# Kernel tuning notes

Measured on AMD Instinct MI355X. Metric: run time of the kernel, lower is better.

Reference implementation:

```python
import jax, jax.numpy as jnp
import numpy as np

Cl, Nl, Cv, Nv, M = 32, 128, 8, 64, 500000


def _sample1d(line, g):
    # line: [C, N]; g in [-1,1]; align_corners=True, zeros padding
    C, N = line.shape
    ix = (g + 1.0) * 0.5 * (N - 1)
    i0 = jnp.floor(ix)
    w = ix - i0
    i0 = i0.astype(jnp.int32)
    def gth(i, wt):
        valid = (i >= 0) & (i < N)
        return line[:, jnp.clip(i, 0, N - 1)] * (wt * valid)
    return (gth(i0, 1.0 - w) + gth(i0 + 1, w)).T  # [M, C]


def _sample2d(plane, gx, gy):
    # plane: [C, H, W]; grid x -> W axis, y -> H axis (torch grid_sample convention)
    C, H, W = plane.shape
    ix = (gx + 1.0) * 0.5 * (W - 1)
    iy = (gy + 1.0) * 0.5 * (H - 1)
    x0 = jnp.floor(ix); y0 = jnp.floor(iy)
    wx = ix - x0; wy = iy - y0
    x0 = x0.astype(jnp.int32); y0 = y0.astype(jnp.int32)
    flat = plane.reshape(C, -1)
    def gth(xi, yi, wt):
        valid = (xi >= 0) & (xi < W) & (yi >= 0) & (yi < H)
        idx = jnp.clip(yi, 0, H - 1) * W + jnp.clip(xi, 0, W - 1)
        return flat[:, idx] * (wt * valid)
    out = (gth(x0, y0, (1 - wx) * (1 - wy)) + gth(x0 + 1, y0, wx * (1 - wy))
           + gth(x0, y0 + 1, (1 - wx) * wy) + gth(x0 + 1, y0 + 1, wx * wy))
    return out.T  # [M, C]


def _sample3d(vol, gx, gy, gz):
    # vol: [C, D, H, W]; grid (x,y,z) -> (W,H,D) axes
    C, D, H, W = vol.shape
    ix = (gx + 1.0) * 0.5 * (W - 1)
    iy = (gy + 1.0) * 0.5 * (H - 1)
    iz = (gz + 1.0) * 0.5 * (D - 1)
    x0 = jnp.floor(ix); y0 = jnp.floor(iy); z0 = jnp.floor(iz)
    wx = ix - x0; wy = iy - y0; wz = iz - z0
    x0 = x0.astype(jnp.int32); y0 = y0.astype(jnp.int32); z0 = z0.astype(jnp.int32)
    flat = vol.reshape(C, -1)
    out = 0.0
    for dz in (0, 1):
        for dy in (0, 1):
            for dx in (0, 1):
                xi, yi, zi = x0 + dx, y0 + dy, z0 + dz
                wt = ((wx if dx else 1 - wx) * (wy if dy else 1 - wy) * (wz if dz else 1 - wz))
                valid = (xi >= 0) & (xi < W) & (yi >= 0) & (yi < H) & (zi >= 0) & (zi < D)
                idx = (jnp.clip(zi, 0, D - 1) * H + jnp.clip(yi, 0, H - 1)) * W + jnp.clip(xi, 0, W - 1)
                out = out + flat[:, idx] * (wt * valid)
    return out.T  # [M, C]


def setup_inputs() -> dict:
    key = jax.random.key(0)
    ks = jax.random.split(key, 16)
    rng, shift = 0.4, 0.1
    coordinates = jax.random.uniform(ks[0], (1, M, 3), minval=-1.0, maxval=1.0)
    line_x = jax.random.uniform(ks[1], (Cl, Nl)) * rng + shift
    line_y = jax.random.uniform(ks[2], (Cl, Nl)) * rng + shift
    line_z = jax.random.uniform(ks[3], (Cl, Nl)) * rng + shift
    plane_xy = jax.random.normal(ks[4], (Cl, Nl, Nl)) * rng + shift
    plane_yz = jax.random.normal(ks[5], (Cl, Nl, Nl)) * rng + shift
    plane_xz = jax.random.normal(ks[6], (Cl, Nl, Nl)) * rng + shift
    volume = jax.random.normal(ks[7], (Cv, Nv, Nv, Nv)) * rng + shift
    def lin(k, fi, fo):
        k1, k2 = jax.random.split(k)
        lim = 1.0 / np.sqrt(fi)
        return (jax.random.uniform(k1, (fi, fo), minval=-lim, maxval=lim),
                jax.random.uniform(k2, (fo,), minval=-lim, maxval=lim))
    Wx, bx = lin(ks[8], Cl, Cl)
    Wy, by = lin(ks[9], Cl, Cl)
    Wz, bz = lin(ks[10], Cl, Cl)
    W1, b1 = lin(ks[11], Cl + Cv, 128)
    W2, b2 = lin(ks[12], 128, 1)
    return dict(coordinates=coordinates, line_x=line_x, line_y=line_y, line_z=line_z,
                plane_xy=plane_xy, plane_yz=plane_yz, plane_xz=plane_xz, volume=volume,
                Wx=Wx, bx=bx, Wy=Wy, by=by, Wz=Wz, bz=bz, W1=W1, b1=b1, W2=W2, b2=b2)


def reference(coordinates, line_x, line_y, line_z, plane_xy, plane_yz, plane_xz, volume,
              Wx, bx, Wy, by, Wz, bz, W1, b1, W2, b2):
    c = coordinates[0]  # [M, 3], batch squeezed like the torch code
    x, y, z = c[:, 0], c[:, 1], c[:, 2]
    x_e = _sample1d(line_x, x)
    y_e = _sample1d(line_y, y)
    z_e = _sample1d(line_z, z)
    xy_e = _sample2d(plane_xy, x, y)
    yz_e = _sample2d(plane_yz, y, z)
    xz_e = _sample2d(plane_xz, x, z)
    xyz_e = _sample3d(volume, x, y, z)
    phi = lambda e, W, b: jax.nn.relu(e) @ W + b  # Sequential(ReLU, Linear)
    yztran = phi(yz_e, Wx, bx)
    xztran = phi(xz_e, Wy, by)
    xytran = phi(xy_e, Wz, bz)
    xtran = phi(x_e, Wx, bx)
    ytran = phi(y_e, Wy, by)
    ztran = phi(z_e, Wz, bz)
    features = xtran * yztran + ytran * xztran + ztran * xytran
    features = jnp.concatenate([features, xyz_e], axis=-1)  # [M, Cl+Cv]
    h = jax.nn.relu(features @ W1 + b1)
    return h @ W2 + b2  # [M, 1]
```

## Files before the change

### kernel.cpp

```cpp
#include <hip/hip_runtime.h>

typedef unsigned short u16;
typedef u16 u16x8 __attribute__((ext_vector_type(8)));
typedef _Float16 half2 __attribute__((ext_vector_type(2)));
typedef _Float16 h8v __attribute__((ext_vector_type(8)));
typedef float f4v __attribute__((ext_vector_type(4)));

union H8 { h8v v; half2 p[4]; };

static __device__ __forceinline__ float bf2f(u16 u) {
    union { unsigned int i; float f; } v;
    v.i = ((unsigned int)u) << 16;
    return v.f;
}
static __device__ __forceinline__ u16 f2bf(float f) {
    union { float f; unsigned int i; } v;
    v.f = f;
    unsigned int x = v.i;
    x += 0x7fffu + ((x >> 16) & 1u);
    return (u16)(x >> 16);
}
static __device__ __forceinline__ float gld(int dt, const void* p, int i) {
    return dt ? ((const float*)p)[i] : bf2f(((const u16*)p)[i]);
}
static __device__ __forceinline__ int detect_dt(const void* coords) {
    u16 v = ((const u16*)coords)[threadIdx.x & 63];
    int e = (v >> 7) & 0xFF;
    bool inr = (e >= 90) && (e <= 126);
    unsigned long long m = __ballot(inr);
    return (__popcll(m) >= 56) ? 0 : 1;
}
static __device__ __forceinline__ half2 pk(float a, float b) {
    return __builtin_bit_cast(half2, __builtin_amdgcn_cvt_pkrtz(a, b));
}

#define WF_OFF        64u
#define PLANES_S_OFF  34304u
#define VOL_S_OFF     3180032u
#define LINES_S_OFF   7374336u
#define PART_OFF      7398912u
#define TOT_OFF       11593216u
#define ORDER_OFF     11609600u

#define NBUCK 4096
#define HBLOCKS 256


static __device__ __forceinline__ int make_key(int dt, const void* coords, int p) {
    float x = gld(dt, coords, p * 3 + 0);
    float y = gld(dt, coords, p * 3 + 1);
    float z = gld(dt, coords, p * 3 + 2);
    int kx = min(max((int)((x + 1.0f) * 8.0f), 0), 15);
    int ky = min(max((int)((y + 1.0f) * 8.0f), 0), 15);
    int kz = min(max((int)((z + 1.0f) * 8.0f), 0), 15);
    return (kz * 16 + ky) * 16 + kx;
}

static __device__ __forceinline__ void weights_work(
    int dt, int r,
    const void* Wx, const void* bx, const void* Wy, const void* by,
    const void* Wz, const void* bz, const void* W1, const void* b1,
    const void* W2, const void* b2, float* wbase)
{
    _Float16* WtH = (_Float16*)wbase;
    float*    bv  = wbase + 1536;
    _Float16* W1H = (_Float16*)(wbase + 1632);
    float*    b1v = wbase + 5728;
    float*    W2v = wbase + 5856;
    float*    b2v = wbase + 5984;
    if (r < 3072) {
        int m = r >> 10, idx = r & 1023;
        int o = idx >> 5, c = idx & 31;
        const void* s = (m == 0) ? Wx : (m == 1) ? Wy : Wz;
        WtH[r] = (_Float16)gld(dt, s, c * 32 + o);
    } else if (r < 3168) {
        int q2 = r - 3072;
        int m = q2 >> 5, c = q2 & 31;
        const void* s = (m == 0) ? bx : (m == 1) ? by : bz;
        bv[q2] = gld(dt, s, c);
    } else if (r < 11360) {
        int idx = r - 3168;
        int j = idx >> 6, i = idx & 63;
        W1H[idx] = (i < 40) ? (_Float16)gld(dt, W1, i * 128 + j) : (_Float16)0.0f;
    } else if (r < 11488) {
        b1v[r - 11360] = gld(dt, b1, r - 11360);
    } else if (r < 11616) {
        W2v[r - 11488] = gld(dt, W2, r - 11488);
    } else if (r == 11616) {
        b2v[0] = gld(dt, b2, 0);
    }
}

__global__ __launch_bounds__(256) void kp_prep_all(
    const void* __restrict__ coords,
    const void* __restrict__ lx, const void* __restrict__ ly,
    const void* __restrict__ lz,
    const void* __restrict__ pxy, const void* __restrict__ pyz,
    const void* __restrict__ pxz, const void* __restrict__ vol,
    const void* __restrict__ Wx, const void* __restrict__ bx,
    const void* __restrict__ Wy, const void* __restrict__ by,
    const void* __restrict__ Wz, const void* __restrict__ bz,
    const void* __restrict__ W1, const void* __restrict__ b1,
    const void* __restrict__ W2, const void* __restrict__ b2,
    float* __restrict__ wbase,
    u16* __restrict__ planes_s, u16* __restrict__ vol_s,
    u16* __restrict__ lines_s, unsigned int* __restrict__ part, int M)
{
    __shared__ unsigned int lh[NBUCK];
    int dt = detect_dt(coords);
    int blk = blockIdx.x;
    if (blk < 1798) {
        int t = blk * 256 + threadIdx.x;
        u16x8 v;
        if (t < 196608) {
            int o = t * 8;
            int pl = o >> 19;
            int r  = o & 524287;
            int pos = r >> 5, c0 = r & 31;
            const void* src = (pl == 0) ? pxy : (pl == 1) ? pyz : pxz;
#pragma unroll
            for (int i = 0; i < 8; ++i)
                v[i] = dt ? f2bf(((const float*)src)[(c0 + i) * 16384 + pos])
                          : ((const u16*)src)[(c0 + i) * 16384 + pos];
            *(u16x8*)(planes_s + o) = v;
        } else if (t < 458752) {
            int pos = t - 196608;
#pragma unroll
            for (int c = 0; c < 8; ++c)
                v[c] = dt ? f2bf(((const float*)vol)[c * 262144 + pos])
                          : ((const u16*)vol)[c * 262144 + pos];
            *(u16x8*)(vol_s + pos * 8) = v;
        } else {
            int o = (t - 458752) * 8;
            int l = o >> 12, rr = o & 4095;
            int pos = rr >> 5, c0 = rr & 31;
            const void* src = (l == 0) ? lx : (l == 1) ? ly : lz;
#pragma unroll
            for (int i = 0; i < 8; ++i)
                v[i] = dt ? f2bf(((const float*)src)[(c0 + i) * 128 + pos])
                          : ((const u16*)src)[(c0 + i) * 128 + pos];
            *(u16x8*)(lines_s + o) = v;
        }
    } else if (blk < 1844) {
        int r = (blk - 1798) * 256 + threadIdx.x;
        weights_work(dt, r, Wx, bx, Wy, by, Wz, bz, W1, b1, W2, b2, wbase);
    } else {
        int b = blk - 1844;
        for (int i = threadIdx.x; i < NBUCK; i += 256) lh[i] = 0u;
        __syncthreads();
        for (int p = b * 256 + threadIdx.x; p < M; p += HBLOCKS * 256)
            atomicAdd(&lh[make_key(dt, coords, p)], 1u);
        __syncthreads();
        for (int i = threadIdx.x; i < NBUCK; i += 256)
            part[b * NBUCK + i] = lh[i];
    }
}

__global__ __launch_bounds__(64) void kp_colscan(
    unsigned int* __restrict__ part, unsigned int* __restrict__ tot)
{
    int bkt = blockIdx.x * 64 + threadIdx.x;
    unsigned int run = 0;
#pragma unroll 8
    for (int k = 0; k < HBLOCKS; ++k) {
        unsigned int v = part[k * NBUCK + bkt];
        part[k * NBUCK + bkt] = run;
        run += v;
    }
    tot[bkt] = run;
}

__global__ __launch_bounds__(256) void kp_scatter_det(
    const void* __restrict__ coords, const unsigned int* __restrict__ part,
    const unsigned int* __restrict__ tot,
    int* __restrict__ order, int M)
{
    __shared__ unsigned int cnt[NBUCK];
    __shared__ unsigned int psum[256];
    int b = blockIdx.x;
    int t = threadIdx.x;
    unsigned int bs[16];
    unsigned int s = 0;
#pragma unroll
    for (int i = 0; i < 16; ++i) {
        bs[i] = tot[t * 16 + i];
        s += bs[i];
    }
    psum[t] = s;
    __syncthreads();
    if (t == 0) {
        unsigned int run = 0;
        for (int i = 0; i < 256; ++i) { unsigned int v = psum[i]; psum[i] = run; run += v; }
    }
    __syncthreads();
    unsigned int run = psum[t];
#pragma unroll
    for (int i = 0; i < 16; ++i) {
        int bkt = t * 16 + i;
        cnt[bkt] = run + part[b * NBUCK + bkt];
        run += bs[i];
    }
    __syncthreads();
    int dt = detect_dt(coords);
    for (int p = b * 256 + t; p < M; p += HBLOCKS * 256) {
        int key = make_key(dt, coords, p);
        unsigned int pos = atomicAdd(&cnt[key], 1u);
        order[pos] = p;
    }
}

struct Samp { int i0, i1; float w0, w1; };

static __device__ __forceinline__ Samp make_samp(float g, int N) {
    float ix = (g + 1.0f) * 0.5f * (float)(N - 1);
    float fl = floorf(ix);
    float w  = ix - fl;
    int i  = (int)fl;
    int i1 = i + 1;
    float v0 = (i  >= 0 && i  < N) ? 1.0f : 0.0f;
    float v1 = (i1 >= 0 && i1 < N) ? 1.0f : 0.0f;
    Samp s;
    s.w0 = (1.0f - w) * v0;
    s.w1 = w * v1;
    s.i0 = min(max(i, 0), N - 1);
    s.i1 = min(max(i1, 0), N - 1);
    return s;
}

#define MFMA16(a, b, c) __builtin_amdgcn_mfma_f32_16x16x32_f16((a), (b), (c), 0, 0, 0)

#define SRE 40
#define SR2 72

static __device__ __forceinline__ void term_mfma(
    int lane, const u16* __restrict__ Ls, const Samp& sl,
    const u16* __restrict__ Ps, const Samp& sa, const Samp& sb,
    const _Float16* __restrict__ Wt, const float* __restrict__ bvt,
    _Float16* El, _Float16* Ep, float (&feat)[4][2][4])
{
    int q = lane >> 4, l15 = lane & 15;
    const u16x8* l0  = (const u16x8*)(Ls + sl.i0 * 32);
    const u16x8* l1  = (const u16x8*)(Ls + sl.i1 * 32);
    const u16x8* p00 = (const u16x8*)(Ps + (sb.i0 * 128 + sa.i0) * 32);
    const u16x8* p01 = (const u16x8*)(Ps + (sb.i0 * 128 + sa.i1) * 32);
    const u16x8* p10 = (const u16x8*)(Ps + (sb.i1 * 128 + sa.i0) * 32);
    const u16x8* p11 = (const u16x8*)(Ps + (sb.i1 * 128 + sa.i1) * 32);
    float w00 = sb.w0 * sa.w0, w01 = sb.w0 * sa.w1;
    float w10 = sb.w1 * sa.w0, w11 = sb.w1 * sa.w1;
#pragma unroll
    for (int cc = 0; cc < 4; ++cc) {
        u16x8 A0 = l0[cc], A1 = l1[cc];
        u16x8 Q00 = p00[cc], Q01 = p01[cc], Q10 = p10[cc], Q11 = p11[cc];
        H8 hl, hp;
#pragma unroll
        for (int kk = 0; kk < 4; ++kk) {
            int k0 = 2 * kk, k1 = k0 + 1;
            float el0 = sl.w0 * bf2f(A0[k0]) + sl.w1 * bf2f(A1[k0]);
            float el1 = sl.w0 * bf2f(A0[k1]) + sl.w1 * bf2f(A1[k1]);
            float ep0 = w00 * bf2f(Q00[k0]) + w01 * bf2f(Q01[k0])
                      + w10 * bf2f(Q10[k0]) + w11 * bf2f(Q11[k0]);
            float ep1 = w00 * bf2f(Q00[k1]) + w01 * bf2f(Q01[k1])
                      + w10 * bf2f(Q10[k1]) + w11 * bf2f(Q11[k1]);
            hl.p[kk] = pk(fmaxf(el0, 0.0f), fmaxf(el1, 0.0f));
            hp.p[kk] = pk(fmaxf(ep0, 0.0f), fmaxf(ep1, 0.0f));
        }
        *(h8v*)&El[lane * SRE + cc * 8] = hl.v;
        *(h8v*)&Ep[lane * SRE + cc * 8] = hp.v;
    }
    __syncthreads();
    h8v bf0 = *(const h8v*)&Wt[(l15) * 32 + q * 8];
    h8v bf1 = *(const h8v*)&Wt[(16 + l15) * 32 + q * 8];
    float bb0 = bvt[l15], bb1 = bvt[16 + l15];
    f4v c0 = {bb0, bb0, bb0, bb0};
    f4v c1 = {bb1, bb1, bb1, bb1};
#pragma unroll
    for (int mt = 0; mt < 4; ++mt) {
        h8v aL = *(const h8v*)&El[(mt * 16 + l15) * SRE + q * 8];
        h8v aP = *(const h8v*)&Ep[(mt * 16 + l15) * SRE + q * 8];
        f4v ta0 = MFMA16(aL, bf0, c0);
        f4v tb0 = MFMA16(aP, bf0, c0);
        f4v ta1 = MFMA16(aL, bf1, c1);
        f4v tb1 = MFMA16(aP, bf1, c1);
#pragma unroll
        for (int r = 0; r < 4; ++r) {
            feat[mt][0][r] += ta0[r] * tb0[r];
            feat[mt][1][r] += ta1[r] * tb1[r];
        }
    }
    __syncthreads();
}

__global__ __launch_bounds__(64) void kp_main_mfma(
    const void* __restrict__ coords, const int* __restrict__ order,
    const u16* __restrict__ planes_s, const u16* __restrict__ vol_s,
    const u16* __restrict__ lines_s,
    const float* __restrict__ wbase,
    void* __restrict__ out, int M)
{
    __shared__ _Float16 eb[5120];
    __shared__ float res[64];
    int dt = detect_dt(coords);
    const _Float16* WtH = (const _Float16*)wbase;
    const float*    bv  = wbase + 1536;
    const _Float16* W1H = (const _Float16*)(wbase + 1632);
    const float*    b1v = wbase + 5728;
    const float*    W2v = wbase + 5856;
    const float*    b2v = wbase + 5984;

    int lane = threadIdx.x;
    int q = lane >> 4, l15 = lane & 15;
    _Float16* El = eb;
    _Float16* Ep = eb + 2560;
    _Float16* E2 = eb;

    int p = blockIdx.x * 64 + lane;
    p = min(p, M - 1);
    int sp = order[p];

    float x = gld(dt, coords, sp * 3 + 0);
    float y = gld(dt, coords, sp * 3 + 1);
    float z = gld(dt, coords, sp * 3 + 2);

    Samp sx = make_samp(x, 128), sy = make_samp(y, 128), sz = make_samp(z, 128);

    float feat[4][2][4];
#pragma unroll
    for (int mt = 0; mt < 4; ++mt)
#pragma unroll
        for (int n = 0; n < 2; ++n)
#pragma unroll
            for (int r = 0; r < 4; ++r) feat[mt][n][r] = 0.0f;

    term_mfma(lane, lines_s + 0 * 4096, sx, planes_s + 1 * 524288, sy, sz,
              WtH + 0,    bv + 0,  El, Ep, feat);
    term_mfma(lane, lines_s + 1 * 4096, sy, planes_s + 2 * 524288, sx, sz,
              WtH + 1024, bv + 32, El, Ep, feat);
    term_mfma(lane, lines_s + 2 * 4096, sz, planes_s + 0 * 524288, sx, sy,
              WtH + 2048, bv + 64, El, Ep, feat);

#pragma unroll
    for (int mt = 0; mt < 4; ++mt)
#pragma unroll
        for (int n = 0; n < 2; ++n)
#pragma unroll
            for (int r = 0; r < 4; ++r)
                E2[(mt * 16 + q * 4 + r) * SR2 + n * 16 + l15] =
                    (_Float16)feat[mt][n][r];
    {
        Samp vx = make_samp(x, 64), vy = make_samp(y, 64), vz = make_samp(z, 64);
        float vf[8];
#pragma unroll
        for (int c = 0; c < 8; ++c) vf[c] = 0.0f;
#pragma unroll
        for (int corner = 0; corner < 8; ++corner) {
            int dx = corner & 1, dy = (corner >> 1) & 1, dz = corner >> 2;
            int xi = dx ? vx.i1 : vx.i0;
            int yi = dy ? vy.i1 : vy.i0;
            int zi = dz ? vz.i1 : vz.i0;
            float w = (dx ? vx.w1 : vx.w0) * (dy ? vy.w1 : vy.w0) * (dz ? vz.w1 : vz.w0);
            u16x8 v = *(const u16x8*)(vol_s + (((zi * 64) + yi) * 64 + xi) * 8);
#pragma unroll
            for (int c = 0; c < 8; ++c)
                vf[c] = fmaf(w, bf2f(v[c]), vf[c]);
        }
        H8 hv;
#pragma unroll
        for (int k = 0; k < 4; ++k) hv.p[k] = pk(vf[2 * k], vf[2 * k + 1]);
        *(h8v*)&E2[lane * SR2 + 32] = hv.v;
        h8v zz = {};
        *(h8v*)&E2[lane * SR2 + 40] = zz;
        *(h8v*)&E2[lane * SR2 + 48] = zz;
        *(h8v*)&E2[lane * SR2 + 56] = zz;
    }
    __syncthreads();

    h8v af[4][2];
#pragma unroll
    for (int mt = 0; mt < 4; ++mt)
#pragma unroll
        for (int ks = 0; ks < 2; ++ks)
            af[mt][ks] = *(const h8v*)&E2[(mt * 16 + l15) * SR2 + ks * 32 + q * 8];

    float s[4][4];
#pragma unroll
    for (int mt = 0; mt < 4; ++mt)
#pragma unroll
        for (int r = 0; r < 4; ++r) s[mt][r] = 0.0f;

#pragma unroll
    for (int NT = 0; NT < 8; ++NT) {
        int o = NT * 16 + l15;
        h8v b0 = *(const h8v*)&W1H[o * 64 + q * 8];
        h8v b1f = *(const h8v*)&W1H[o * 64 + 32 + q * 8];
        float w2 = W2v[o];
        float bb = b1v[o];
        f4v cinit = {bb, bb, bb, bb};
#pragma unroll
        for (int mt = 0; mt < 4; ++mt) {
            f4v c = MFMA16(af[mt][0], b0, cinit);
            c = MFMA16(af[mt][1], b1f, c);
#pragma unroll
            for (int r = 0; r < 4; ++r)
                s[mt][r] = fmaf(fmaxf(c[r], 0.0f), w2, s[mt][r]);
        }
    }
#pragma unroll
    for (int mt = 0; mt < 4; ++mt)
#pragma unroll
        for (int r = 0; r < 4; ++r) {
            float v = s[mt][r];
            v += __shfl_xor(v, 1);
            v += __shfl_xor(v, 2);
            v += __shfl_xor(v, 4);
            v += __shfl_xor(v, 8);
            s[mt][r] = v;
        }
    if (l15 == 0) {
#pragma unroll
        for (int mt = 0; mt < 4; ++mt)
#pragma unroll
            for (int r = 0; r < 4; ++r)
                res[mt * 16 + q * 4 + r] = s[mt][r];
    }
    __syncthreads();
    float rr = res[lane] + b2v[0];
    if (dt) ((float*)out)[sp] = rr;
    else    ((u16*)out)[sp] = f2bf(rr);
}

__global__ void kp_prep_weights_fb(
    const void* __restrict__ coords,
    const void* __restrict__ Wx, const void* __restrict__ bx,
    const void* __restrict__ Wy, const void* __restrict__ by,
    const void* __restrict__ Wz, const void* __restrict__ bz,
    const void* __restrict__ W1, const void* __restrict__ b1,
    const void* __restrict__ W2, const void* __restrict__ b2,
    float* __restrict__ wbase)
{
    int dt = detect_dt(coords);
    int t = blockIdx.x * blockDim.x + threadIdx.x;
    weights_work(dt, t, Wx, bx, Wy, by, Wz, bz, W1, b1, W2, b2, wbase);
}

__global__ __launch_bounds__(256) void kp_main_direct(
    const void* __restrict__ coords,
    const void* __restrict__ lx, const void* __restrict__ ly, const void* __restrict__ lz,
    const void* __restrict__ pxy, const void* __restrict__ pyz, const void* __restrict__ pxz,
    const void* __restrict__ vol,
    const float* __restrict__ wbase,
    void* __restrict__ out, int M)
{
    int dt = detect_dt(coords);
    const _Float16* WtH = (const _Float16*)wbase;
    const float*    bv  = wbase + 1536;
    const _Float16* W1H = (const _Float16*)(wbase + 1632);
    const float*    b1v = wbase + 5728;
    const float*    W2v = wbase + 5856;
    const float*    b2v = wbase + 5984;

    int p = blockIdx.x * 256 + threadIdx.x;
    p = min(p, M - 1);

    float x = gld(dt, coords, p * 3 + 0);
    float y = gld(dt, coords, p * 3 + 1);
    float z = gld(dt, coords, p * 3 + 2);

    Samp sx = make_samp(x, 128), sy = make_samp(y, 128), sz = make_samp(z, 128);

    float feat[40];
#pragma unroll
    for (int o = 0; o < 40; ++o) feat[o] = 0.0f;

    const void* Ls[3] = {lx, ly, lz};
    const void* Psv[3] = {pyz, pxz, pxy};
    Samp sl3[3] = {sx, sy, sz};
    Samp sa3[3] = {sy, sx, sx};
    Samp sb3[3] = {sz, sz, sy};
#pragma unroll 1
    for (int m = 0; m < 3; ++m) {
        float ta[32], tb[32];
        const float* bvt = bv + m * 32;
        const _Float16* Wt = WtH + m * 1024;
#pragma unroll
        for (int o = 0; o < 32; ++o) { ta[o] = bvt[o]; tb[o] = bvt[o]; }
        Samp sl = sl3[m], sa = sa3[m], sb = sb3[m];
        float w00 = sb.w0 * sa.w0, w01 = sb.w0 * sa.w1;
        float w10 = sb.w1 * sa.w0, w11 = sb.w1 * sa.w1;
        int i00 = sb.i0 * 128 + sa.i0, i01 = sb.i0 * 128 + sa.i1;
        int i10 = sb.i1 * 128 + sa.i0, i11 = sb.i1 * 128 + sa.i1;
#pragma unroll 1
        for (int c = 0; c < 32; ++c) {
            float el = sl.w0 * gld(dt, Ls[m], c * 128 + sl.i0)
                     + sl.w1 * gld(dt, Ls[m], c * 128 + sl.i1);
            float ep = w00 * gld(dt, Psv[m], c * 16384 + i00)
                     + w01 * gld(dt, Psv[m], c * 16384 + i01)
                     + w10 * gld(dt, Psv[m], c * 16384 + i10)
                     + w11 * gld(dt, Psv[m], c * 16384 + i11);
            float r1 = fmaxf(el, 0.0f), r2 = fmaxf(ep, 0.0f);
#pragma unroll
            for (int o = 0; o < 32; ++o) {
                float w = (float)Wt[o * 32 + c];
                ta[o] = fmaf(r1, w, ta[o]);
                tb[o] = fmaf(r2, w, tb[o]);
            }
        }
#pragma unroll
        for (int o = 0; o < 32; ++o) feat[o] = fmaf(ta[o], tb[o], feat[o]);
    }

    Samp vx = make_samp(x, 64), vy = make_samp(y, 64), vz = make_samp(z, 64);
#pragma unroll 1
    for (int corner = 0; corner < 8; ++corner) {
        int dx = corner & 1, dy = (corner >> 1) & 1, dz = corner >> 2;
        int xi = dx ? vx.i1 : vx.i0;
        int yi = dy ? vy.i1 : vy.i0;
        int zi = dz ? vz.i1 : vz.i0;
        float w = (dx ? vx.w1 : vx.w0) * (dy ? vy.w1 : vy.w0) * (dz ? vz.w1 : vz.w0);
        int pos = ((zi * 64) + yi) * 64 + xi;
#pragma unroll
        for (int c = 0; c < 8; ++c)
            feat[32 + c] = fmaf(w, gld(dt, vol, c * 262144 + pos), feat[32 + c]);
    }

    float acc_out = b2v[0];
#pragma unroll 2
    for (int j = 0; j < 128; ++j) {
        float acc = b1v[j];
        const _Float16* wr = W1H + j * 64;
#pragma unroll
        for (int i = 0; i < 40; ++i)
            acc = fmaf(feat[i], (float)wr[i], acc);
        acc_out = fmaf(fmaxf(acc, 0.0f), W2v[j], acc_out);
    }
    if (dt) ((float*)out)[p] = acc_out;
    else    ((u16*)out)[p] = f2bf(acc_out);
}

extern "C" void kernel_launch(void* const* d_in, const int* in_sizes, int n_in,
                              void* d_out, int out_size, void* d_ws, size_t ws_size,
                              hipStream_t stream) {
    const void* coords = d_in[0];
    const void* lx  = d_in[1];
    const void* ly  = d_in[2];
    const void* lz  = d_in[3];
    const void* pxy = d_in[4];
    const void* pyz = d_in[5];
    const void* pxz = d_in[6];
    const void* vol = d_in[7];
    const void* Wx  = d_in[8];
    const void* bx  = d_in[9];
    const void* Wy  = d_in[10];
    const void* by  = d_in[11];
    const void* Wz  = d_in[12];
    const void* bz  = d_in[13];
    const void* W1  = d_in[14];
    const void* b1  = d_in[15];
    const void* W2  = d_in[16];
    const void* b2  = d_in[17];

    int M = in_sizes[0] / 3;

    char* ws = (char*)d_ws;
    float*        wbase    = (float*)(ws + WF_OFF);
    u16*          planes_s = (u16*)(ws + PLANES_S_OFF);
    u16*          vol_s    = (u16*)(ws + VOL_S_OFF);
    u16*          lines_s  = (u16*)(ws + LINES_S_OFF);
    unsigned int* part     = (unsigned int*)(ws + PART_OFF);
    unsigned int* tot      = (unsigned int*)(ws + TOT_OFF);
    int*          order    = (int*)(ws + ORDER_OFF);

    size_t need_sorted = (size_t)ORDER_OFF + (size_t)M * 4u;

    if (ws_size >= need_sorted) {
        kp_prep_all<<<2100, 256, 0, stream>>>(coords, lx, ly, lz, pxy, pyz, pxz, vol,
                                              Wx, bx, Wy, by, Wz, bz, W1, b1, W2, b2,
                                              wbase, planes_s, vol_s, lines_s, part, M);
        kp_colscan<<<64, 64, 0, stream>>>(part, tot);
        kp_scatter_det<<<HBLOCKS, 256, 0, stream>>>(coords, part, tot, order, M);
        int blocks64 = (M + 63) / 64;
        kp_main_mfma<<<blocks64, 64, 0, stream>>>(coords, order, planes_s, vol_s,
                                                  lines_s, wbase, d_out, M);
    } else {
        int blocks = (M + 255) / 256;
        kp_prep_weights_fb<<<46, 256, 0, stream>>>(coords, Wx, bx, Wy, by, Wz, bz,
                                                   W1, b1, W2, b2, wbase);
        kp_main_direct<<<blocks, 256, 0, stream>>>(coords, lx, ly, lz, pxy, pyz, pxz,
                                                   vol, wbase, d_out, M);
    }
}
```

Measured before the change: 203.7 us.

## Scatter coordinates into sorted order, shrink histogram partials, swizzle block order

```diff
diff --git a/kernel.cpp b/kernel.cpp
--- a/kernel.cpp
+++ b/kernel.cpp
@@ -39,21 +39,22 @@
 #define VOL_S_OFF     3180032u
 #define LINES_S_OFF   7374336u
 #define PART_OFF      7398912u
-#define TOT_OFF       11593216u
-#define ORDER_OFF     11609600u
+#define TOT_OFF       9496064u
+#define ORDER_OFF     9512448u
 
 #define NBUCK 4096
 #define HBLOCKS 256
 
 
-static __device__ __forceinline__ int make_key(int dt, const void* coords, int p) {
-    float x = gld(dt, coords, p * 3 + 0);
-    float y = gld(dt, coords, p * 3 + 1);
-    float z = gld(dt, coords, p * 3 + 2);
+static __device__ __forceinline__ int make_key3(float x, float y, float z) {
     int kx = min(max((int)((x + 1.0f) * 8.0f), 0), 15);
     int ky = min(max((int)((y + 1.0f) * 8.0f), 0), 15);
     int kz = min(max((int)((z + 1.0f) * 8.0f), 0), 15);
     return (kz * 16 + ky) * 16 + kx;
+}
+static __device__ __forceinline__ int make_key(int dt, const void* coords, int p) {
+    return make_key3(gld(dt, coords, p * 3 + 0), gld(dt, coords, p * 3 + 1),
+                     gld(dt, coords, p * 3 + 2));
 }
 
 static __device__ __forceinline__ void weights_work(
@@ -104,7 +105,7 @@
     const void* __restrict__ W2, const void* __restrict__ b2,
     float* __restrict__ wbase,
     u16* __restrict__ planes_s, u16* __restrict__ vol_s,
-    u16* __restrict__ lines_s, unsigned int* __restrict__ part, int M)
+    u16* __restrict__ lines_s, u16* __restrict__ part, int M)
 {
     __shared__ unsigned int lh[NBUCK];
     int dt = detect_dt(coords);
@@ -152,28 +153,28 @@
             atomicAdd(&lh[make_key(dt, coords, p)], 1u);
         __syncthreads();
         for (int i = threadIdx.x; i < NBUCK; i += 256)
-            part[b * NBUCK + i] = lh[i];
+            part[b * NBUCK + i] = (u16)lh[i];
     }
 }
 
 __global__ __launch_bounds__(64) void kp_colscan(
-    unsigned int* __restrict__ part, unsigned int* __restrict__ tot)
+    u16* __restrict__ part, unsigned int* __restrict__ tot)
 {
     int bkt = blockIdx.x * 64 + threadIdx.x;
     unsigned int run = 0;
 #pragma unroll 8
     for (int k = 0; k < HBLOCKS; ++k) {
         unsigned int v = part[k * NBUCK + bkt];
-        part[k * NBUCK + bkt] = run;
+        part[k * NBUCK + bkt] = (u16)run;
         run += v;
     }
     tot[bkt] = run;
 }
 
 __global__ __launch_bounds__(256) void kp_scatter_det(
-    const void* __restrict__ coords, const unsigned int* __restrict__ part,
+    const void* __restrict__ coords, const u16* __restrict__ part,
     const unsigned int* __restrict__ tot,
-    int* __restrict__ order, int M)
+    int* __restrict__ order, u16* __restrict__ scoords, int M)
 {
     __shared__ unsigned int cnt[NBUCK];
     __shared__ unsigned int psum[256];
@@ -197,15 +198,24 @@
 #pragma unroll
     for (int i = 0; i < 16; ++i) {
         int bkt = t * 16 + i;
-        cnt[bkt] = run + part[b * NBUCK + bkt];
+        cnt[bkt] = run + (unsigned int)part[b * NBUCK + bkt];
         run += bs[i];
     }
     __syncthreads();
     int dt = detect_dt(coords);
+    const u16* cu = (const u16*)coords;
     for (int p = b * 256 + t; p < M; p += HBLOCKS * 256) {
-        int key = make_key(dt, coords, p);
+        float x = gld(dt, coords, p * 3 + 0);
+        float y = gld(dt, coords, p * 3 + 1);
+        float z = gld(dt, coords, p * 3 + 2);
+        int key = make_key3(x, y, z);
         unsigned int pos = atomicAdd(&cnt[key], 1u);
         order[pos] = p;
+        if (dt == 0) {
+            scoords[pos * 3 + 0] = cu[p * 3 + 0];
+            scoords[pos * 3 + 1] = cu[p * 3 + 1];
+            scoords[pos * 3 + 2] = cu[p * 3 + 2];
+        }
     }
 }
 
@@ -292,6 +302,7 @@
 
 __global__ __launch_bounds__(64) void kp_main_mfma(
     const void* __restrict__ coords, const int* __restrict__ order,
+    const u16* __restrict__ scoords,
     const u16* __restrict__ planes_s, const u16* __restrict__ vol_s,
     const u16* __restrict__ lines_s,
     const float* __restrict__ wbase,
@@ -313,13 +324,23 @@
     _Float16* Ep = eb + 2560;
     _Float16* E2 = eb;
 
-    int p = blockIdx.x * 64 + lane;
+    int chunk = gridDim.x >> 3;
+    int bsw = (blockIdx.x & 7) * chunk + (blockIdx.x >> 3);
+
+    int p = bsw * 64 + lane;
     p = min(p, M - 1);
     int sp = order[p];
 
-    float x = gld(dt, coords, sp * 3 + 0);
-    float y = gld(dt, coords, sp * 3 + 1);
-    float z = gld(dt, coords, sp * 3 + 2);
+    float x, y, z;
+    if (dt == 0) {
+        x = bf2f(scoords[p * 3 + 0]);
+        y = bf2f(scoords[p * 3 + 1]);
+        z = bf2f(scoords[p * 3 + 2]);
+    } else {
+        x = ((const float*)coords)[sp * 3 + 0];
+        y = ((const float*)coords)[sp * 3 + 1];
+        z = ((const float*)coords)[sp * 3 + 2];
+    }
 
     Samp sx = make_samp(x, 128), sy = make_samp(y, 128), sz = make_samp(z, 128);
 
@@ -565,20 +586,24 @@
     u16*          planes_s = (u16*)(ws + PLANES_S_OFF);
     u16*          vol_s    = (u16*)(ws + VOL_S_OFF);
     u16*          lines_s  = (u16*)(ws + LINES_S_OFF);
-    unsigned int* part     = (unsigned int*)(ws + PART_OFF);
+    u16*          part     = (u16*)(ws + PART_OFF);
     unsigned int* tot      = (unsigned int*)(ws + TOT_OFF);
     int*          order    = (int*)(ws + ORDER_OFF);
-
-    size_t need_sorted = (size_t)ORDER_OFF + (size_t)M * 4u;
+    u16*          scoords  = (u16*)(ws + ORDER_OFF + (size_t)M * 4u);
+
+    size_t need_sorted = (size_t)ORDER_OFF + (size_t)M * 4u + (size_t)M * 6u;
 
     if (ws_size >= need_sorted) {
         kp_prep_all<<<2100, 256, 0, stream>>>(coords, lx, ly, lz, pxy, pyz, pxz, vol,
                                               Wx, bx, Wy, by, Wz, bz, W1, b1, W2, b2,
                                               wbase, planes_s, vol_s, lines_s, part, M);
         kp_colscan<<<64, 64, 0, stream>>>(part, tot);
-        kp_scatter_det<<<HBLOCKS, 256, 0, stream>>>(coords, part, tot, order, M);
+        kp_scatter_det<<<HBLOCKS, 256, 0, stream>>>(coords, part, tot, order,
+                                                    scoords, M);
         int blocks64 = (M + 63) / 64;
-        kp_main_mfma<<<blocks64, 64, 0, stream>>>(coords, order, planes_s, vol_s,
+        blocks64 = (blocks64 + 7) & ~7;
+        kp_main_mfma<<<blocks64, 64, 0, stream>>>(coords, order, scoords,
+                                                  planes_s, vol_s,
                                                   lines_s, wbase, d_out, M);
     } else {
         int blocks = (M + 255) / 256;
```

After: 202.7 us. About the same (-0.5%).
